# Performance work log

Hardware: AMD Instinct MI355X
Metric: run time of the kernel (lower is better)

The kernel has to match this reference:

```python
import jax, jax.numpy as jnp
import numpy as np

TOP_K = 2

def setup_inputs() -> dict:
    key = jax.random.key(0)
    k0, k1, k2, k3, k4 = jax.random.split(key, 5)
    B, S, D, H, E = 2, 2048, 1024, 2048, 8
    x = jax.random.normal(k0, (B, S, D), dtype=jnp.float32)
    router_w = jax.random.normal(k1, (D, E), dtype=jnp.float32) * (1.0 / np.sqrt(D))
    wg = jax.random.normal(k2, (E, D, H), dtype=jnp.float32) * (1.0 / np.sqrt(D))
    wu = jax.random.normal(k3, (E, D, H), dtype=jnp.float32) * (1.0 / np.sqrt(D))
    wd = jax.random.normal(k4, (E, H, D), dtype=jnp.float32) * (1.0 / np.sqrt(H))
    return {"x": x, "router_w": router_w, "wg": wg, "wu": wu, "wd": wd}

def reference(x, router_w, wg, wu, wd):
    B, S, D = x.shape
    E = router_w.shape[1]
    xf = x.reshape(-1, D)                                   # [T, D]
    router_logits = xf @ router_w                           # [T, E]
    top_logits, top_idx = jax.lax.top_k(router_logits, TOP_K)
    top_w = jax.nn.softmax(top_logits, axis=-1)             # [T, k]
    # Dense combine weights: W[t, e] = routing weight if e in top-k of t, else 0.
    combine = jnp.sum(jax.nn.one_hot(top_idx, E, dtype=x.dtype) * top_w[..., None], axis=1)  # [T, E]
    # SwiGLU experts, computed for all tokens and masked by the combine weights
    # (mathematically identical to the gather/scatter form in the original).
    gate = jnp.einsum('td,edh->eth', xf, wg)                # [E, T, H]
    up = jnp.einsum('td,edh->eth', xf, wu)                  # [E, T, H]
    fused = jax.nn.silu(gate) * up                          # [E, T, H]
    expert_out = jnp.einsum('eth,ehd->etd', fused, wd)      # [E, T, D]
    y = jnp.einsum('etd,te->td', expert_out, combine)       # [T, D]
    return y.reshape(B, S, D)
```

## Files before the change

kernel.cpp:

```cpp
#include <hip/hip_runtime.h>
#include <hip/hip_bf16.h>

#define T_TOK 4096
#define DDIM  1024
#define HDIM  2048
#define NEXP  8
#define MAXSLOT 9216

typedef __attribute__((ext_vector_type(4))) float f32x4;
typedef __attribute__((ext_vector_type(8))) short s16x8;
typedef __hip_bfloat16 bf16;

typedef const void __attribute__((address_space(1))) gvoid;
typedef void __attribute__((address_space(3))) svoid;

__device__ __forceinline__ void gload16(const void* g, void* l) {
    __builtin_amdgcn_global_load_lds((gvoid*)g, (svoid*)l, 16, 0, 0);
}

__device__ __forceinline__ int sw_r(int r) { return ((r >> 2) ^ ((r & 3) << 2)) & 15; }

__global__ void prep_kernel(const float* __restrict__ x, const float* __restrict__ rw,
                            const float* __restrict__ wg, const float* __restrict__ wu,
                            const float* __restrict__ wd,
                            bf16* __restrict__ wguT, bf16* __restrict__ wdT,
                            int* __restrict__ r_e, float* __restrict__ r_w,
                            bf16* __restrict__ xb, float* __restrict__ y) {
    int bid = blockIdx.x;
    int tid = threadIdx.x;

    if (bid >= 12288) {
        int rb = bid - 12288;
        {
            float4 z4 = {0.f, 0.f, 0.f, 0.f};
            size_t ybase = (size_t)rb * 4096 + tid * 4;
#pragma unroll
            for (int i = 0; i < 4; ++i)
                *reinterpret_cast<float4*>(y + ybase + (size_t)i * 1024) = z4;
        }
        int wave = tid >> 6, lane = tid & 63;
        int t = rb * 4 + wave;
        const float* xr = x + (size_t)t * DDIM;
        bf16* xbr = xb + (size_t)t * DDIM;
        double acc[NEXP];
#pragma unroll
        for (int e = 0; e < NEXP; ++e) acc[e] = 0.0;
#pragma unroll
        for (int c = 0; c < 4; ++c) {
            int d = c * 256 + lane * 4;
            float4 v = *reinterpret_cast<const float4*>(xr + d);
            union { ushort4 u; bf16 h[4]; } o;
            o.h[0] = __float2bfloat16(v.x);
            o.h[1] = __float2bfloat16(v.y);
            o.h[2] = __float2bfloat16(v.z);
            o.h[3] = __float2bfloat16(v.w);
            *reinterpret_cast<ushort4*>(xbr + d) = o.u;
            const float* rw0 = rw + (size_t)d * NEXP;
#pragma unroll
            for (int j = 0; j < 4; ++j) {
                float xv = (&v.x)[j];
                const float* rwr = rw0 + j * NEXP;
#pragma unroll
                for (int e = 0; e < NEXP; ++e) acc[e] += (double)xv * (double)rwr[e];
            }
        }
#pragma unroll
        for (int e = 0; e < NEXP; ++e) {
#pragma unroll
            for (int off = 32; off > 0; off >>= 1) acc[e] += __shfl_down(acc[e], off);
        }
        if (lane == 0) {
            int i0 = 0; double v0 = acc[0];
#pragma unroll
            for (int e = 1; e < NEXP; ++e) if (acc[e] > v0) { v0 = acc[e]; i0 = e; }
            int i1 = -1; double v1 = -1e300;
#pragma unroll
            for (int e = 0; e < NEXP; ++e) { if (e == i0) continue; if (acc[e] > v1) { v1 = acc[e]; i1 = e; } }
            float w0 = 1.0f / (1.0f + expf((float)(v1 - v0)));
            float w1 = 1.0f - w0;
            r_e[2*t]   = i0; r_e[2*t+1] = i1;
            r_w[2*t]   = w0; r_w[2*t+1] = w1;
        }
        return;
    }

    __shared__ __align__(16) bf16 tile[64 * 64];
    const float* inp; bf16* outp; int C, OS, r0, c0;
    if (bid < 8192) {
        int z = bid >> 9;
        int t = bid & 511;
        int which = z >> 3, e = z & 7;
        inp = (which ? wu : wg) + (size_t)e * DDIM * HDIM;
        outp = wguT + (size_t)e * 2 * HDIM * DDIM + (size_t)which * DDIM;
        C = HDIM; OS = 2 * DDIM;
        r0 = (t >> 5) * 64;
        c0 = (t & 31) * 64;
    } else {
        int b2 = bid - 8192;
        int e = b2 >> 9;
        int t = b2 & 511;
        inp = wd + (size_t)e * HDIM * DDIM;
        outp = wdT + (size_t)e * DDIM * HDIM;
        C = DDIM; OS = HDIM;
        r0 = (t >> 4) * 64;
        c0 = (t & 15) * 64;
    }
#pragma unroll
    for (int i = 0; i < 4; ++i) {
        int idx = i * 256 + tid;
        int r = idx >> 4, c4 = (idx & 15) * 4;
        float4 v = *reinterpret_cast<const float4*>(inp + (size_t)(r0 + r) * C + c0 + c4);
        union { ushort4 u; bf16 h[4]; } o;
        o.h[0] = __float2bfloat16(v.x);
        o.h[1] = __float2bfloat16(v.y);
        o.h[2] = __float2bfloat16(v.z);
        o.h[3] = __float2bfloat16(v.w);
        *reinterpret_cast<ushort4*>(&tile[r * 64 + 4 * ((c4 >> 2) ^ sw_r(r))]) = o.u;
    }
    __syncthreads();
#pragma unroll
    for (int i = 0; i < 4; ++i) {
        int idx = i * 256 + tid;
        int c = idx >> 4, r4 = (idx & 15) * 4;
        int g = c >> 2, ce = c & 3;
        union { ushort4 u; bf16 h[4]; } w;
#pragma unroll
        for (int j = 0; j < 4; ++j) {
            int r = r4 + j;
            w.h[j] = tile[r * 64 + 4 * (g ^ sw_r(r)) + ce];
        }
        *reinterpret_cast<ushort4*>(outp + (size_t)(c0 + c) * OS + r0 + r4) = w.u;
    }
}

__global__ void binning_kernel(const int* __restrict__ r_e, const float* __restrict__ r_w,
                               int* __restrict__ offs, int* __restrict__ cnt,
                               int* __restrict__ list, float* __restrict__ slot_w) {
    __shared__ int scnt[NEXP], scur[NEXP], soff[NEXP + 1];
    int tid = threadIdx.x;
    if (tid < NEXP) { scnt[tid] = 0; scur[tid] = 0; }
    __syncthreads();
    for (int i = tid; i < 2 * T_TOK; i += 1024) atomicAdd(&scnt[r_e[i]], 1);
    __syncthreads();
    if (tid == 0) {
        int s = 0;
        for (int e = 0; e < NEXP; ++e) { soff[e] = s; s += (scnt[e] + 127) & ~127; }
        soff[NEXP] = s;
    }
    __syncthreads();
    if (tid < NEXP + 1) offs[tid] = soff[tid];
    if (tid < NEXP) cnt[tid] = scnt[tid];
    for (int i = tid; i < 2 * T_TOK; i += 1024) {
        int e = r_e[i];
        int pos = atomicAdd(&scur[e], 1);
        int slot = soff[e] + pos;
        list[slot] = i >> 1;
        slot_w[slot] = r_w[i];
    }
}

__device__ __forceinline__ int find_expert(const int* offs, int slot0) {
    int e = 0;
#pragma unroll
    for (int i = 0; i < NEXP - 1; ++i) e += (offs[e + 1] <= slot0) ? 1 : 0;
    return e;
}

__global__ __launch_bounds__(512, 2)
void gateup_kernel(const bf16* __restrict__ xb, const bf16* __restrict__ wguT,
                   const int* __restrict__ offs, const int* __restrict__ cnt,
                   const int* __restrict__ list, bf16* __restrict__ hbuf) {
    int slot0 = blockIdx.y * 128;
    if (slot0 >= offs[NEXP]) return;
    int e = find_expert(offs, slot0);
    int base = offs[e];
    int ne = cnt[e];
    int m0 = slot0 - base;
    int n0 = blockIdx.x * 128;

    __shared__ bf16 As[2][8192];
    __shared__ bf16 Bs[2][8192];

    int tid = threadIdx.x, lane = tid & 63, wid = tid >> 6;
    int sub = lane >> 3;
    int koff = 8 * ((lane & 7) ^ sub);

    const bf16* bbase = wguT + (size_t)e * (2 * HDIM) * DDIM + (size_t)n0 * DDIM;

    const bf16* aS[2]; const bf16* bS[2];
    int sdst[2];
#pragma unroll
    for (int j = 0; j < 2; ++j) {
        int q = wid + j * 8;
        int row = q * 8 + sub;
        int r = m0 + row; if (r > ne - 1) r = ne - 1;
        aS[j] = xb + (size_t)list[base + r] * DDIM + koff;
        bS[j] = bbase + (size_t)row * DDIM + koff;
        sdst[j] = q * 512;
    }

    int rl = lane & 15, kq = 8 * (lane >> 4);
    int wrow = (wid >> 2) * 64;
    int wcol = (wid & 3) * 32;
    int xorv = (rl & 7) * 8;

    f32x4 zero4 = {0.f, 0.f, 0.f, 0.f};
    f32x4 acc[4][2];
#pragma unroll
    for (int mi = 0; mi < 4; ++mi) { acc[mi][0] = zero4; acc[mi][1] = zero4; }

    const int nk = DDIM / 64;

#define GU_STAGE(tt, buf)                                     \
    {                                                         \
        int k0 = (tt) * 64;                                   \
        gload16(aS[0] + k0, &As[buf][sdst[0]]);               \
        gload16(aS[1] + k0, &As[buf][sdst[1]]);               \
        gload16(bS[0] + k0, &Bs[buf][sdst[0]]);               \
        gload16(bS[1] + k0, &Bs[buf][sdst[1]]);               \
    }

#define GU_COMPUTE(Ab, Bb)                                                        \
    _Pragma("unroll")                                                             \
    for (int kk = 0; kk < 2; ++kk) {                                              \
        int kos = (kk * 32 + kq) ^ xorv;                                          \
        s16x8 a[4], b[2];                                                         \
        _Pragma("unroll")                                                         \
        for (int mi = 0; mi < 4; ++mi)                                            \
            a[mi] = *reinterpret_cast<const s16x8*>(&(Ab)[(wrow + mi * 16 + rl) * 64 + kos]); \
        _Pragma("unroll")                                                         \
        for (int ni = 0; ni < 2; ++ni)                                            \
            b[ni] = *reinterpret_cast<const s16x8*>(&(Bb)[(wcol + ni * 16 + rl) * 64 + kos]); \
        __builtin_amdgcn_s_setprio(1);                                            \
        _Pragma("unroll")                                                         \
        for (int mi = 0; mi < 4; ++mi)                                            \
            _Pragma("unroll")                                                     \
            for (int ni = 0; ni < 2; ++ni)                                        \
                acc[mi][ni] = __builtin_amdgcn_mfma_f32_16x16x32_bf16(a[mi], b[ni], acc[mi][ni], 0, 0, 0); \
        __builtin_amdgcn_s_setprio(0);                                            \
    }

    GU_STAGE(0, 0);
    GU_STAGE(1, 1);

    for (int t = 0; t < nk; ++t) {
        if (t + 1 < nk) asm volatile("s_waitcnt vmcnt(4)" ::: "memory");
        else            asm volatile("s_waitcnt vmcnt(0)" ::: "memory");
        __builtin_amdgcn_s_barrier();
        GU_COMPUTE(As[t & 1], Bs[t & 1]);
        __builtin_amdgcn_sched_barrier(0);
        __builtin_amdgcn_s_barrier();
        if (t + 2 < nk) GU_STAGE(t + 2, t & 1);
    }
#undef GU_COMPUTE
#undef GU_STAGE

    int rbase = (lane >> 4) * 4, cbase = lane & 15;
    bool evenlane = (lane & 1) == 0;
#pragma unroll
    for (int mi = 0; mi < 4; ++mi) {
#pragma unroll
        for (int ni = 0; ni < 2; ++ni) {
#pragma unroll
            for (int r = 0; r < 4; ++r) {
                float own = acc[mi][ni][r];
                float oth = __shfl_xor(own, 1);
                int row = m0 + wrow + mi * 16 + rbase + r;
                if (evenlane && row < ne) {
                    float g = own, u = oth;
                    float h = (g / (1.0f + expf(-g))) * u;
                    int hcol = (n0 + wcol + ni * 16 + cbase) >> 1;
                    hbuf[(size_t)(base + row) * HDIM + hcol] = __float2bfloat16(h);
                }
            }
        }
    }
}

__global__ __launch_bounds__(512, 2)
void down_kernel(const bf16* __restrict__ hbuf, const bf16* __restrict__ wdT,
                 const int* __restrict__ offs, const int* __restrict__ cnt,
                 const int* __restrict__ list, const float* __restrict__ slot_w,
                 float* __restrict__ y) {
    int slot0 = blockIdx.y * 128;
    if (slot0 >= offs[NEXP]) return;
    int e = find_expert(offs, slot0);
    int base = offs[e];
    int ne = cnt[e];
    int m0 = slot0 - base;
    int n0 = blockIdx.x * 128;

    __shared__ bf16 As[2][8192];
    __shared__ bf16 Bs[2][8192];

    int tid = threadIdx.x, lane = tid & 63, wid = tid >> 6;
    int sub = lane >> 3;
    int koff = 8 * ((lane & 7) ^ sub);

    const bf16* bbase = wdT + (size_t)e * DDIM * HDIM + (size_t)n0 * HDIM;

    const bf16* aS[2]; const bf16* bS[2];
    int sdst[2];
#pragma unroll
    for (int j = 0; j < 2; ++j) {
        int q = wid + j * 8;
        int row = q * 8 + sub;
        int r = m0 + row; if (r > ne - 1) r = ne - 1;
        aS[j] = hbuf + (size_t)(base + r) * HDIM + koff;
        bS[j] = bbase + (size_t)row * HDIM + koff;
        sdst[j] = q * 512;
    }

    int rl = lane & 15, kq = 8 * (lane >> 4);
    int wrow = (wid >> 2) * 64;
    int wcol = (wid & 3) * 32;
    int xorv = (rl & 7) * 8;

    f32x4 zero4 = {0.f, 0.f, 0.f, 0.f};
    f32x4 acc[4][2];
#pragma unroll
    for (int mi = 0; mi < 4; ++mi) { acc[mi][0] = zero4; acc[mi][1] = zero4; }

    const int nk = HDIM / 64;

#define DN_STAGE(tt, buf)                                     \
    {                                                         \
        int k0 = (tt) * 64;                                   \
        gload16(aS[0] + k0, &As[buf][sdst[0]]);               \
        gload16(aS[1] + k0, &As[buf][sdst[1]]);               \
        gload16(bS[0] + k0, &Bs[buf][sdst[0]]);               \
        gload16(bS[1] + k0, &Bs[buf][sdst[1]]);               \
    }

#define DN_COMPUTE(Ab, Bb)                                                        \
    _Pragma("unroll")                                                             \
    for (int kk = 0; kk < 2; ++kk) {                                              \
        int kos = (kk * 32 + kq) ^ xorv;                                          \
        s16x8 a[4], b[2];                                                         \
        _Pragma("unroll")                                                         \
        for (int mi = 0; mi < 4; ++mi)                                            \
            a[mi] = *reinterpret_cast<const s16x8*>(&(Ab)[(wrow + mi * 16 + rl) * 64 + kos]); \
        _Pragma("unroll")                                                         \
        for (int ni = 0; ni < 2; ++ni)                                            \
            b[ni] = *reinterpret_cast<const s16x8*>(&(Bb)[(wcol + ni * 16 + rl) * 64 + kos]); \
        __builtin_amdgcn_s_setprio(1);                                            \
        _Pragma("unroll")                                                         \
        for (int mi = 0; mi < 4; ++mi)                                            \
            _Pragma("unroll")                                                     \
            for (int ni = 0; ni < 2; ++ni)                                        \
                acc[mi][ni] = __builtin_amdgcn_mfma_f32_16x16x32_bf16(a[mi], b[ni], acc[mi][ni], 0, 0, 0); \
        __builtin_amdgcn_s_setprio(0);                                            \
    }

    DN_STAGE(0, 0);
    DN_STAGE(1, 1);

    for (int t = 0; t < nk; ++t) {
        if (t + 1 < nk) asm volatile("s_waitcnt vmcnt(4)" ::: "memory");
        else            asm volatile("s_waitcnt vmcnt(0)" ::: "memory");
        __builtin_amdgcn_s_barrier();
        DN_COMPUTE(As[t & 1], Bs[t & 1]);
        __builtin_amdgcn_sched_barrier(0);
        __builtin_amdgcn_s_barrier();
        if (t + 2 < nk) DN_STAGE(t + 2, t & 1);
    }
#undef DN_COMPUTE
#undef DN_STAGE

    int rbase = (lane >> 4) * 4, cbase = lane & 15;
#pragma unroll
    for (int mi = 0; mi < 4; ++mi) {
#pragma unroll
        for (int r = 0; r < 4; ++r) {
            int row = m0 + wrow + mi * 16 + rbase + r;
            if (row < ne) {
                int slot = base + row;
                int tok = list[slot];
                float w = slot_w[slot];
                float* yrow = y + (size_t)tok * DDIM + n0 + wcol + cbase;
#pragma unroll
                for (int ni = 0; ni < 2; ++ni)
                    atomicAdd(yrow + ni * 16, w * acc[mi][ni][r]);
            }
        }
    }
}

extern "C" void kernel_launch(void* const* d_in, const int* in_sizes, int n_in,
                              void* d_out, int out_size, void* d_ws, size_t ws_size,
                              hipStream_t stream) {
    const float* x  = (const float*)d_in[0];
    const float* rw = (const float*)d_in[1];
    const float* wg = (const float*)d_in[2];
    const float* wu = (const float*)d_in[3];
    const float* wd = (const float*)d_in[4];
    float* y = (float*)d_out;

    char* ws = (char*)d_ws;
    int*   r_e    = (int*)  (ws + 0);
    float* r_w    = (float*)(ws + 32768);
    int*   offs   = (int*)  (ws + 65600);
    int*   cnt    = (int*)  (ws + 65640);
    int*   list   = (int*)  (ws + 65792);
    float* slot_w = (float*)(ws + 65792 + 4 * MAXSLOT);
    bf16*  xb     = (bf16*) (ws + 1048576ull);
    bf16*  wguT   = (bf16*) (ws + 16777216ull);
    bf16*  wdT    = (bf16*) (ws + 83886080ull);
    bf16*  hbuf   = (bf16*) (ws + 117440512ull);

    prep_kernel<<<dim3(13312), 256, 0, stream>>>(x, rw, wg, wu, wd, wguT, wdT,
                                                 r_e, r_w, xb, y);
    binning_kernel<<<dim3(1), 1024, 0, stream>>>(r_e, r_w, offs, cnt, list, slot_w);

    gateup_kernel<<<dim3(2 * HDIM / 128, MAXSLOT / 128, 1), 512, 0, stream>>>(
        xb, wguT, offs, cnt, list, hbuf);
    down_kernel<<<dim3(DDIM / 128, MAXSLOT / 128, 1), 512, 0, stream>>>(
        hbuf, wdT, offs, cnt, list, slot_w, y);
}
```

Baseline: 278.0 us.

## Move down-projection weight transpose into gate/up GEMM launch to overlap

Measured after the change: 269.3 us, median of 2. -3.1%, faster.

```diff
diff --git a/kernel.cpp b/kernel.cpp
--- a/kernel.cpp
+++ b/kernel.cpp
@@ -6,6 +6,8 @@
 #define HDIM  2048
 #define NEXP  8
 #define MAXSLOT 9216
+#define GU_YTILES 72
+#define WD_YROWS 64
 
 typedef __attribute__((ext_vector_type(4))) float f32x4;
 typedef __attribute__((ext_vector_type(8))) short s16x8;
@@ -22,15 +24,14 @@
 
 __global__ void prep_kernel(const float* __restrict__ x, const float* __restrict__ rw,
                             const float* __restrict__ wg, const float* __restrict__ wu,
-                            const float* __restrict__ wd,
-                            bf16* __restrict__ wguT, bf16* __restrict__ wdT,
+                            bf16* __restrict__ wguT,
                             int* __restrict__ r_e, float* __restrict__ r_w,
                             bf16* __restrict__ xb, float* __restrict__ y) {
     int bid = blockIdx.x;
     int tid = threadIdx.x;
 
-    if (bid >= 12288) {
-        int rb = bid - 12288;
+    if (bid >= 8192) {
+        int rb = bid - 8192;
         {
             float4 z4 = {0.f, 0.f, 0.f, 0.f};
             size_t ybase = (size_t)rb * 4096 + tid * 4;
@@ -85,31 +86,18 @@
     }
 
     __shared__ __align__(16) bf16 tile[64 * 64];
-    const float* inp; bf16* outp; int C, OS, r0, c0;
-    if (bid < 8192) {
-        int z = bid >> 9;
-        int t = bid & 511;
-        int which = z >> 3, e = z & 7;
-        inp = (which ? wu : wg) + (size_t)e * DDIM * HDIM;
-        outp = wguT + (size_t)e * 2 * HDIM * DDIM + (size_t)which * DDIM;
-        C = HDIM; OS = 2 * DDIM;
-        r0 = (t >> 5) * 64;
-        c0 = (t & 31) * 64;
-    } else {
-        int b2 = bid - 8192;
-        int e = b2 >> 9;
-        int t = b2 & 511;
-        inp = wd + (size_t)e * HDIM * DDIM;
-        outp = wdT + (size_t)e * DDIM * HDIM;
-        C = DDIM; OS = HDIM;
-        r0 = (t >> 4) * 64;
-        c0 = (t & 15) * 64;
-    }
+    int z = bid >> 9;
+    int t = bid & 511;
+    int which = z >> 3, e = z & 7;
+    const float* inp = (which ? wu : wg) + (size_t)e * DDIM * HDIM;
+    bf16* outp = wguT + (size_t)e * 2 * HDIM * DDIM + (size_t)which * DDIM;
+    int r0 = (t >> 5) * 64;
+    int c0 = (t & 31) * 64;
 #pragma unroll
     for (int i = 0; i < 4; ++i) {
         int idx = i * 256 + tid;
         int r = idx >> 4, c4 = (idx & 15) * 4;
-        float4 v = *reinterpret_cast<const float4*>(inp + (size_t)(r0 + r) * C + c0 + c4);
+        float4 v = *reinterpret_cast<const float4*>(inp + (size_t)(r0 + r) * HDIM + c0 + c4);
         union { ushort4 u; bf16 h[4]; } o;
         o.h[0] = __float2bfloat16(v.x);
         o.h[1] = __float2bfloat16(v.y);
@@ -129,7 +117,7 @@
             int r = r4 + j;
             w.h[j] = tile[r * 64 + 4 * (g ^ sw_r(r)) + ce];
         }
-        *reinterpret_cast<ushort4*>(outp + (size_t)(c0 + c) * OS + r0 + r4) = w.u;
+        *reinterpret_cast<ushort4*>(outp + (size_t)(c0 + c) * (2 * DDIM) + r0 + r4) = w.u;
     }
 }
 
@@ -169,7 +157,56 @@
 __global__ __launch_bounds__(512, 2)
 void gateup_kernel(const bf16* __restrict__ xb, const bf16* __restrict__ wguT,
                    const int* __restrict__ offs, const int* __restrict__ cnt,
-                   const int* __restrict__ list, bf16* __restrict__ hbuf) {
+                   const int* __restrict__ list, bf16* __restrict__ hbuf,
+                   const float* __restrict__ wd, bf16* __restrict__ wdT) {
+    __shared__ bf16 As[2][8192];
+    __shared__ bf16 Bs[2][8192];
+
+    int tid = threadIdx.x;
+
+    if (blockIdx.y >= GU_YTILES) {
+        int wdid = (blockIdx.y - GU_YTILES) * 32 + blockIdx.x;
+        bf16* tile = &As[0][0];
+#pragma unroll
+        for (int tt = 0; tt < 2; ++tt) {
+            int tb = wdid * 2 + tt;
+            int e = tb >> 9;
+            int t = tb & 511;
+            const float* inp = wd + (size_t)e * HDIM * DDIM;
+            bf16* outp = wdT + (size_t)e * DDIM * HDIM;
+            int r0 = (t >> 4) * 64;
+            int c0 = (t & 15) * 64;
+#pragma unroll
+            for (int i = 0; i < 2; ++i) {
+                int idx = i * 512 + tid;
+                int r = idx >> 4, c4 = (idx & 15) * 4;
+                float4 v = *reinterpret_cast<const float4*>(inp + (size_t)(r0 + r) * DDIM + c0 + c4);
+                union { ushort4 u; bf16 h[4]; } o;
+                o.h[0] = __float2bfloat16(v.x);
+                o.h[1] = __float2bfloat16(v.y);
+                o.h[2] = __float2bfloat16(v.z);
+                o.h[3] = __float2bfloat16(v.w);
+                *reinterpret_cast<ushort4*>(&tile[r * 64 + 4 * ((c4 >> 2) ^ sw_r(r))]) = o.u;
+            }
+            __syncthreads();
+#pragma unroll
+            for (int i = 0; i < 2; ++i) {
+                int idx = i * 512 + tid;
+                int c = idx >> 4, r4 = (idx & 15) * 4;
+                int g = c >> 2, ce = c & 3;
+                union { ushort4 u; bf16 h[4]; } w;
+#pragma unroll
+                for (int j = 0; j < 4; ++j) {
+                    int r = r4 + j;
+                    w.h[j] = tile[r * 64 + 4 * (g ^ sw_r(r)) + ce];
+                }
+                *reinterpret_cast<ushort4*>(outp + (size_t)(c0 + c) * HDIM + r0 + r4) = w.u;
+            }
+            __syncthreads();
+        }
+        return;
+    }
+
     int slot0 = blockIdx.y * 128;
     if (slot0 >= offs[NEXP]) return;
     int e = find_expert(offs, slot0);
@@ -178,10 +215,7 @@
     int m0 = slot0 - base;
     int n0 = blockIdx.x * 128;
 
-    __shared__ bf16 As[2][8192];
-    __shared__ bf16 Bs[2][8192];
-
-    int tid = threadIdx.x, lane = tid & 63, wid = tid >> 6;
+    int lane = tid & 63, wid = tid >> 6;
     int sub = lane >> 3;
     int koff = 8 * ((lane & 7) ^ sub);
 
@@ -408,12 +442,11 @@
     bf16*  wdT    = (bf16*) (ws + 83886080ull);
     bf16*  hbuf   = (bf16*) (ws + 117440512ull);
 
-    prep_kernel<<<dim3(13312), 256, 0, stream>>>(x, rw, wg, wu, wd, wguT, wdT,
-                                                 r_e, r_w, xb, y);
+    prep_kernel<<<dim3(9216), 256, 0, stream>>>(x, rw, wg, wu, wguT, r_e, r_w, xb, y);
     binning_kernel<<<dim3(1), 1024, 0, stream>>>(r_e, r_w, offs, cnt, list, slot_w);
 
-    gateup_kernel<<<dim3(2 * HDIM / 128, MAXSLOT / 128, 1), 512, 0, stream>>>(
-        xb, wguT, offs, cnt, list, hbuf);
+    gateup_kernel<<<dim3(2 * HDIM / 128, GU_YTILES + WD_YROWS, 1), 512, 0, stream>>>(
+        xb, wguT, offs, cnt, list, hbuf, wd, wdT);
     down_kernel<<<dim3(DDIM / 128, MAXSLOT / 128, 1), 512, 0, stream>>>(
         hbuf, wdT, offs, cnt, list, slot_w, y);
 }
```
